# Kernel tuning notes

Measured on AMD Instinct MI355X. Metric: run time of the kernel, lower is better.

## Reference

```python
import jax, jax.numpy as jnp
import numpy as np

H = 4        # num_heads
DH = 64      # output_dim (d_head)
D = 256      # input_dim (hidden)
NUM_LAYERS = 2


def _gru_cell(x, h, Wih, Whh, bih, bhh):
    # PyTorch GRUCell: gates ordered (r, z, n)
    gi = x @ Wih.T + bih
    gh = h @ Whh.T + bhh
    i_r, i_z, i_n = jnp.split(gi, 3, axis=-1)
    h_r, h_z, h_n = jnp.split(gh, 3, axis=-1)
    r = jax.nn.sigmoid(i_r + h_r)
    z = jax.nn.sigmoid(i_z + h_z)
    n = jnp.tanh(i_n + r * h_n)
    return (1.0 - z) * n + z * h


def _mha(x, attn_mask, Wq, bq, Wk, bk, Wv, bv, Wo):
    B, N, _ = x.shape
    q = (x @ Wq.T + bq).reshape(B, N, H, DH)
    k = (x @ Wk.T + bk).reshape(B, N, H, DH)
    v = (x @ Wv.T + bv).reshape(B, N, H, DH)
    # scores computed in fp32 (autocast disabled in original)
    scores = jnp.einsum('bnhd,bmhd->bhnm', q.astype(jnp.float32), k.astype(jnp.float32)) / jnp.float32(DH) ** 0.5
    scores = jnp.where(attn_mask[:, None], jnp.float32(-1e9), scores)  # mask broadcast over heads
    attn = jax.nn.softmax(scores, axis=-1)
    ctx = jnp.einsum('bhnm,bmhd->bnhd', attn, v).reshape(B, N, H * DH)
    return ctx @ Wo.T  # W_O has no bias


def setup_inputs() -> dict:
    B, N = 1024, 128
    key = jax.random.key(0)
    ks = jax.random.split(key, 14)
    s = 0.02
    return {
        'latent': jax.random.normal(ks[0], (B, N, D), jnp.float32),
        'comm_mask': jax.random.randint(ks[1], (B, N, N), 0, 2) > 0,
        'trait_weight': jax.random.normal(ks[2], (B, N), jnp.float32),
        'Wq': jax.random.normal(ks[3], (H * DH, D), jnp.float32) * s,
        'bq': jnp.zeros((H * DH,), jnp.float32),
        'Wk': jax.random.normal(ks[4], (H * DH, D), jnp.float32) * s,
        'bk': jnp.zeros((H * DH,), jnp.float32),
        'Wv': jax.random.normal(ks[5], (H * DH, D), jnp.float32) * s,
        'bv': jnp.zeros((H * DH,), jnp.float32),
        'Wo': jax.random.normal(ks[6], (DH, H * DH), jnp.float32) * s,
        'Wih': jax.random.normal(ks[7], (3 * D, DH), jnp.float32) * s,
        'Whh': jax.random.normal(ks[8], (3 * D, D), jnp.float32) * s,
        'bih': jnp.zeros((3 * D,), jnp.float32),
        'bhh': jnp.zeros((3 * D,), jnp.float32),
    }


def reference(latent, comm_mask, trait_weight, Wq, bq, Wk, bk, Wv, bv, Wo, Wih, Whh, bih, bhh):
    B, N, _ = latent.shape
    attn_mask = ~comm_mask                                    # [B,N,N] True = blocked
    update_mask = (comm_mask.sum(axis=-1) > 1)[..., None]     # [B,N,1]
    for _ in range(NUM_LAYERS):
        info = _mha(latent, attn_mask, Wq, bq, Wk, bk, Wv, bv, Wo)          # [B,N,DH]
        upd = _gru_cell(info.reshape(-1, DH), latent.reshape(-1, D), Wih, Whh, bih, bhh)
        latent = jnp.where(update_mask, upd.reshape(B, N, D), latent)
    return latent
```

## Files before the change

kernel.cpp:

```cpp
#include <hip/hip_runtime.h>
#include <stdint.h>

#define NTOK 128
#define DHID 256
#define NHEAD 4
#define DHEAD 64

typedef short bf16x8 __attribute__((ext_vector_type(8)));
typedef float f32x4 __attribute__((ext_vector_type(4)));

#define MFMA(a,b,c) __builtin_amdgcn_mfma_f32_16x16x32_bf16((a),(b),(c),0,0,0)

__device__ __forceinline__ float bf2f(uint16_t u){
  union { uint32_t i; float f; } v; v.i = ((uint32_t)u) << 16; return v.f;
}
__device__ __forceinline__ uint16_t f2bf(float f){
  union { uint32_t i; float f; } v; v.f = f;
  uint32_t i = v.i + 0x7FFFu + ((v.i >> 16) & 1u);
  return (uint16_t)(i >> 16);
}

__global__ void k_detect(const uint32_t* __restrict__ raw, uint32_t* __restrict__ flag){
  int lane = threadIdx.x;
  int hits = 0;
  #pragma unroll
  for (int i = 0; i < 16; i++){
    uint32_t w = raw[lane*16 + i];
    uint32_t e = (w >> 7) & 0xFFu;
    hits += (e >= 0x70u && e <= 0x8Fu) ? 1 : 0;
  }
  #pragma unroll
  for (int m = 1; m < 64; m <<= 1) hits += __shfl_xor(hits, m);
  if (lane == 0) *flag = (hits > 512) ? 1u : 0u;
}

__global__ void k_conv(const void* __restrict__ src, unsigned long long off,
                       uint16_t* __restrict__ dst, const uint32_t* __restrict__ flag, int n){
  const int isbf = (int)*flag;
  int i0 = (blockIdx.x * blockDim.x + threadIdx.x) * 8;
  int stride = gridDim.x * blockDim.x * 8;
  if (isbf){
    const uint16_t* s = (const uint16_t*)src + off;
    for (int i = i0; i < n; i += stride)
      *(bf16x8*)(dst + i) = *(const bf16x8*)(s + i);
  } else {
    const float* s = (const float*)src + off;
    for (int i = i0; i < n; i += stride){
      float4 a = *(const float4*)(s + i);
      float4 b = *(const float4*)(s + i + 4);
      uint16_t o[8] = {f2bf(a.x),f2bf(a.y),f2bf(a.z),f2bf(a.w),
                       f2bf(b.x),f2bf(b.y),f2bf(b.z),f2bf(b.w)};
      *(bf16x8*)(dst + i) = *(const bf16x8*)o;
    }
  }
}

__global__ void k_store(const uint16_t* __restrict__ L, void* __restrict__ dst,
                        unsigned long long off, const uint32_t* __restrict__ flag, int n){
  const int isbf = (int)*flag;
  int i0 = (blockIdx.x * blockDim.x + threadIdx.x) * 8;
  int stride = gridDim.x * blockDim.x * 8;
  if (isbf){
    uint16_t* d = (uint16_t*)dst + off;
    for (int i = i0; i < n; i += stride)
      *(bf16x8*)(d + i) = *(const bf16x8*)(L + i);
  } else {
    float* d = (float*)dst + off;
    for (int i = i0; i < n; i += stride){
      bf16x8 v = *(const bf16x8*)(L + i);
      #pragma unroll
      for (int e = 0; e < 8; e++) d[i + e] = bf2f((uint16_t)v[e]);
    }
  }
}

__global__ __launch_bounds__(256) void k_maskpack(const int* __restrict__ mask,
                                                  unsigned long long* __restrict__ packed,
                                                  unsigned char* __restrict__ upd, int nrows){
  int row = blockIdx.x * 4 + (threadIdx.x >> 6);
  if (row >= nrows) return;
  int lane = threadIdx.x & 63;
  const int* mrow = mask + (size_t)row * NTOK;
  unsigned long long b0 = __ballot(mrow[lane] != 0);
  unsigned long long b1 = __ballot(mrow[lane + 64] != 0);
  if (lane == 0){
    packed[row*2 + 0] = b0;
    packed[row*2 + 1] = b1;
    upd[row] = (unsigned char)((__popcll(b0) + __popcll(b1)) > 1 ? 1 : 0);
  }
}

__global__ __launch_bounds__(256) void k_qkv(
    const uint16_t* __restrict__ X,
    const uint16_t* __restrict__ Wq, const uint16_t* __restrict__ bq,
    const uint16_t* __restrict__ Wk, const uint16_t* __restrict__ bk,
    const uint16_t* __restrict__ Wv, const uint16_t* __restrict__ bv,
    uint16_t* __restrict__ Oq, uint16_t* __restrict__ Ok, uint16_t* __restrict__ Ov)
{
  extern __shared__ uint16_t sm[];
  uint16_t* Xs = sm;
  uint16_t* Ws = sm + 64*256;
  const int r0 = blockIdx.x * 64;
  const int tid = threadIdx.x;
  const int lane = tid & 63, lr = lane & 15, lg = lane >> 4;
  const int wav = tid >> 6;
  const int wr = (wav >> 1) * 32, wc = (wav & 1) * 32;

  #pragma unroll
  for (int i = 0; i < 8; i++){
    int c = tid + i*256, row = c >> 5, g = c & 31;
    *(bf16x8*)(Xs + row*256 + (g ^ (row & 7))*8) =
        *(const bf16x8*)(X + (size_t)(r0+row)*DHID + g*8);
  }

  bf16x8 wreg[8];
  auto wptr = [&](int t)->const uint16_t*{
    int w = t >> 2;
    return (w == 0) ? Wq : ((w == 1) ? Wk : Wv);
  };
  auto preload = [&](int t){
    const uint16_t* W = wptr(t);
    int c0t = (t & 3) * 64;
    #pragma unroll
    for (int i = 0; i < 8; i++){
      int idx = tid + i*256, r = idx >> 5, g = idx & 31;
      wreg[i] = *(const bf16x8*)(W + (size_t)(c0t + r)*DHID + g*8);
    }
  };
  preload(0);

  for (int t = 0; t < 12; t++){
    __syncthreads();
    #pragma unroll
    for (int i = 0; i < 8; i++){
      int idx = tid + i*256, r = idx >> 5, g = idx & 31;
      *(bf16x8*)(Ws + r*256 + ((g ^ (r & 7))*8)) = wreg[i];
    }
    __syncthreads();
    if (t < 11) preload(t+1);

    f32x4 acc[2][2] = {};
    #pragma unroll
    for (int kk = 0; kk < 8; kk++){
      int off = ((kk*4 + lg) ^ (lr & 7)) * 8;
      bf16x8 a0 = *(const bf16x8*)(Xs + (wr +      lr)*256 + off);
      bf16x8 a1 = *(const bf16x8*)(Xs + (wr + 16 + lr)*256 + off);
      bf16x8 b0 = *(const bf16x8*)(Ws + (wc +      lr)*256 + off);
      bf16x8 b1 = *(const bf16x8*)(Ws + (wc + 16 + lr)*256 + off);
      acc[0][0] = MFMA(a0, b0, acc[0][0]);
      acc[0][1] = MFMA(a0, b1, acc[0][1]);
      acc[1][0] = MFMA(a1, b0, acc[1][0]);
      acc[1][1] = MFMA(a1, b1, acc[1][1]);
    }
    int w = t >> 2, c0t = (t & 3) * 64;
    const uint16_t* bias = (w == 0) ? bq : ((w == 1) ? bk : bv);
    uint16_t* O = (w == 0) ? Oq : ((w == 1) ? Ok : Ov);
    #pragma unroll
    for (int i = 0; i < 2; i++)
    #pragma unroll
    for (int j = 0; j < 2; j++){
      int col = c0t + wc + j*16 + lr;
      float bvv = bf2f(bias[col]);
      #pragma unroll
      for (int rr = 0; rr < 4; rr++){
        int row = r0 + wr + i*16 + lg*4 + rr;
        O[(size_t)row*DHID + col] = f2bf(acc[i][j][rr] + bvv);
      }
    }
  }
}

__global__ __launch_bounds__(256) void k_attn(
    const uint16_t* __restrict__ Q, const uint16_t* __restrict__ Kb, const uint16_t* __restrict__ V,
    const unsigned long long* __restrict__ packed, uint16_t* __restrict__ ctx)
{
  extern __shared__ uint16_t sm[];
  uint16_t* Ks = sm;
  uint16_t* Vt = sm + 128*64;
  uint16_t* Ps = Vt + 64*128;
  const int b = blockIdx.x >> 2;
  const int h = blockIdx.x & 3;
  const int tid = threadIdx.x, lane = tid & 63, wav = tid >> 6;
  const int lr = lane & 15, lg = lane >> 4;
  const size_t base = ((size_t)b * NTOK) * DHID + h * DHEAD;

  #pragma unroll
  for (int i = 0; i < 4; i++){
    int c = tid + i*256;
    int row = c >> 3, g = c & 7;
    *(bf16x8*)(Ks + row*64 + (g ^ (row & 7))*8) =
        *(const bf16x8*)(Kb + base + (size_t)row*DHID + g*8);
  }
  #pragma unroll
  for (int i = 0; i < 4; i++){
    int c = tid + i*256;
    int n = c & 127, d8 = (c >> 7) * 8;
    bf16x8 v = *(const bf16x8*)(V + base + (size_t)n*DHID + d8);
    #pragma unroll
    for (int e = 0; e < 8; e++){
      int d = d8 + e;
      Vt[d*128 + ((n >> 3) ^ (d & 7))*8 + (n & 7)] = (uint16_t)v[e];
    }
  }
  __syncthreads();

  const int qrow0 = wav * 32;
  bf16x8 qf[2][2];
  #pragma unroll
  for (int i = 0; i < 2; i++)
  #pragma unroll
  for (int kk = 0; kk < 2; kk++)
    qf[i][kk] = *(const bf16x8*)(Q + base + (size_t)(qrow0 + i*16 + lr)*DHID + kk*32 + lg*8);

  f32x4 sa[2][8] = {};
  #pragma unroll
  for (int kk = 0; kk < 2; kk++){
    int off = ((kk*4 + lg) ^ (lr & 7)) * 8;
    #pragma unroll
    for (int j = 0; j < 8; j++){
      bf16x8 bf = *(const bf16x8*)(Ks + (j*16 + lr)*64 + off);
      sa[0][j] = MFMA(qf[0][kk], bf, sa[0][j]);
      sa[1][j] = MFMA(qf[1][kk], bf, sa[1][j]);
    }
  }
  #pragma unroll
  for (int i = 0; i < 2; i++){
    #pragma unroll
    for (int rr = 0; rr < 4; rr++){
      int n = qrow0 + i*16 + lg*4 + rr;
      unsigned long long m0 = packed[((size_t)b*NTOK + n)*2 + 0];
      unsigned long long m1 = packed[((size_t)b*NTOK + n)*2 + 1];
      float sv[8];
      float mx = -3.0e38f;
      #pragma unroll
      for (int j = 0; j < 8; j++){
        int col = j*16 + lr;
        unsigned long long w = (col < 64) ? m0 : m1;
        float s = sa[i][j][rr] * 0.125f;
        sv[j] = ((w >> (col & 63)) & 1ull) ? s : -1e9f;
        mx = fmaxf(mx, sv[j]);
      }
      mx = fmaxf(mx, __shfl_xor(mx, 1));
      mx = fmaxf(mx, __shfl_xor(mx, 2));
      mx = fmaxf(mx, __shfl_xor(mx, 4));
      mx = fmaxf(mx, __shfl_xor(mx, 8));
      float sum = 0.f;
      #pragma unroll
      for (int j = 0; j < 8; j++){ sv[j] = __expf(sv[j] - mx); sum += sv[j]; }
      sum += __shfl_xor(sum, 1);
      sum += __shfl_xor(sum, 2);
      sum += __shfl_xor(sum, 4);
      sum += __shfl_xor(sum, 8);
      float inv = __builtin_amdgcn_rcpf(sum);
      #pragma unroll
      for (int j = 0; j < 8; j++){
        int col = j*16 + lr;
        Ps[n*128 + ((col >> 3) ^ (n & 7))*8 + (col & 7)] = f2bf(sv[j] * inv);
      }
    }
  }
  __syncthreads();

  f32x4 oa[2][4] = {};
  #pragma unroll
  for (int kk = 0; kk < 4; kk++){
    int off = ((kk*4 + lg) ^ (lr & 7)) * 8;
    bf16x8 a0 = *(const bf16x8*)(Ps + (qrow0 +      lr)*128 + off);
    bf16x8 a1 = *(const bf16x8*)(Ps + (qrow0 + 16 + lr)*128 + off);
    #pragma unroll
    for (int j = 0; j < 4; j++){
      bf16x8 bf = *(const bf16x8*)(Vt + (j*16 + lr)*128 + off);
      oa[0][j] = MFMA(a0, bf, oa[0][j]);
      oa[1][j] = MFMA(a1, bf, oa[1][j]);
    }
  }
  #pragma unroll
  for (int i = 0; i < 2; i++)
  #pragma unroll
  for (int j = 0; j < 4; j++)
  #pragma unroll
  for (int rr = 0; rr < 4; rr++){
    int n = qrow0 + i*16 + lg*4 + rr;
    ctx[((size_t)b*NTOK + n)*DHID + h*DHEAD + j*16 + lr] = f2bf(oa[i][j][rr]);
  }
}

__global__ __launch_bounds__(256, 2) void k_gru(
    const uint16_t* __restrict__ ctxp, const uint16_t* __restrict__ lat,
    const uint16_t* __restrict__ Wo, const uint16_t* __restrict__ Wih, const uint16_t* __restrict__ Whh,
    const uint16_t* __restrict__ bih, const uint16_t* __restrict__ bhh,
    const unsigned char* __restrict__ upd, uint16_t* __restrict__ lat_out)
{
  extern __shared__ uint16_t sm[];
  uint16_t* Wb0   = sm;
  uint16_t* Wb1   = sm + 15360;
  uint16_t* Is    = sm + 30720;
  uint16_t* biasS = sm + 38912;
  const int r0 = blockIdx.x * 128;
  const int tid = threadIdx.x, lane = tid & 63, wav = tid >> 6;
  const int lr = lane & 15, lg = lane >> 4;
  const int wrow = wav * 32;

  #pragma unroll
  for (int i = 0; i < 6; i++){
    int idx = tid + i*256;
    if (idx < 1536) biasS[idx] = (idx < 768) ? bih[idx] : bhh[idx - 768];
  }

  auto stage_async = [&](int cs, uint16_t* buf){
    #pragma unroll
    for (int c = 0; c < 7; c++){
      int G = c*256 + tid;
      const uint16_t* src;
      if (G < 1536){
        int r = G >> 5, gp = G & 31;
        src = Whh + (size_t)((r>>4)*256 + cs*16 + (r&15))*DHID + (gp ^ (r&7))*8;
      } else {
        int G2 = G - 1536, r = G2 >> 3, gp = G2 & 7;
        src = Wih + (size_t)((r>>4)*256 + cs*16 + (r&15))*DHEAD + (gp ^ (r&7))*8;
      }
      __builtin_amdgcn_global_load_lds(
          (const __attribute__((address_space(1))) uint32_t*)src,
          (__attribute__((address_space(3))) uint32_t*)(buf + (size_t)G*8),
          16, 0, 0);
    }
    if (tid < 128){
      int G = 1792 + tid;
      int G2 = G - 1536, r = G2 >> 3, gp = G2 & 7;
      const uint16_t* src = Wih + (size_t)((r>>4)*256 + cs*16 + (r&15))*DHEAD + (gp ^ (r&7))*8;
      __builtin_amdgcn_global_load_lds(
          (const __attribute__((address_space(1))) uint32_t*)src,
          (__attribute__((address_space(3))) uint32_t*)(buf + (size_t)G*8),
          16, 0, 0);
    }
  };

  stage_async(0, Wb0);

  f32x4 ai[2][4] = {};
  #pragma unroll
  for (int kk = 0; kk < 8; kk++){
    bf16x8 bw[4];
    #pragma unroll
    for (int j = 0; j < 4; j++)
      bw[j] = *(const bf16x8*)(Wo + (size_t)(j*16 + lr)*DHID + kk*32 + lg*8);
    #pragma unroll
    for (int t = 0; t < 2; t++){
      bf16x8 ac = *(const bf16x8*)(ctxp + (size_t)(r0 + wrow + t*16 + lr)*DHID + kk*32 + lg*8);
      #pragma unroll
      for (int j = 0; j < 4; j++) ai[t][j] = MFMA(ac, bw[j], ai[t][j]);
    }
  }
  #pragma unroll
  for (int t = 0; t < 2; t++)
  #pragma unroll
  for (int j = 0; j < 4; j++)
  #pragma unroll
  for (int rr = 0; rr < 4; rr++){
    int row = wrow + t*16 + lg*4 + rr, col = j*16 + lr;
    Is[row*64 + ((col>>3) ^ (row&7))*8 + (col&7)] = f2bf(ai[t][j][rr]);
  }

  bf16x8 aL[2][8];
  #pragma unroll
  for (int t = 0; t < 2; t++)
  #pragma unroll
  for (int kk = 0; kk < 8; kk++)
    aL[t][kk] = *(const bf16x8*)(lat + (size_t)(r0 + wrow + t*16 + lr)*DHID + kk*32 + lg*8);

  uint32_t u4[2];
  #pragma unroll
  for (int t = 0; t < 2; t++)
    u4[t] = *(const uint32_t*)(upd + r0 + wrow + t*16 + lg*4);

  __syncthreads();

  const float LOG2E = 1.44269504f;
  for (int cs = 0; cs < 16; cs++){
    uint16_t* Wcur = (cs & 1) ? Wb1 : Wb0;
    if (cs < 15) stage_async(cs+1, (cs & 1) ? Wb0 : Wb1);

    const uint16_t* WhhS = Wcur;
    const uint16_t* WihS = Wcur + 12288;

    f32x4 arz[2][2] = {};
    f32x4 gin[2] = {}, ghn[2] = {};

    #pragma unroll
    for (int kk = 0; kk < 2; kk++){
      int off = ((kk*4 + lg) ^ (lr & 7)) * 8;
      bf16x8 br = *(const bf16x8*)(WihS + (0*16 + lr)*64 + off);
      bf16x8 bz = *(const bf16x8*)(WihS + (1*16 + lr)*64 + off);
      bf16x8 bn = *(const bf16x8*)(WihS + (2*16 + lr)*64 + off);
      #pragma unroll
      for (int t = 0; t < 2; t++){
        bf16x8 a = *(const bf16x8*)(Is + (wrow + t*16 + lr)*64 + off);
        arz[0][t] = MFMA(a, br, arz[0][t]);
        arz[1][t] = MFMA(a, bz, arz[1][t]);
        gin[t]    = MFMA(a, bn, gin[t]);
      }
    }
    #pragma unroll
    for (int kk = 0; kk < 8; kk++){
      int off = ((kk*4 + lg) ^ (lr & 7)) * 8;
      bf16x8 br = *(const bf16x8*)(WhhS + (0*16 + lr)*256 + off);
      bf16x8 bz = *(const bf16x8*)(WhhS + (1*16 + lr)*256 + off);
      bf16x8 bn = *(const bf16x8*)(WhhS + (2*16 + lr)*256 + off);
      #pragma unroll
      for (int t = 0; t < 2; t++){
        arz[0][t] = MFMA(aL[t][kk], br, arz[0][t]);
        arz[1][t] = MFMA(aL[t][kk], bz, arz[1][t]);
        ghn[t]    = MFMA(aL[t][kk], bn, ghn[t]);
      }
    }

    int col = cs*16 + lr;
    float brz0 = bf2f(biasS[col])     + bf2f(biasS[768+col]);
    float brz1 = bf2f(biasS[256+col]) + bf2f(biasS[1024+col]);
    float bin_ = bf2f(biasS[512+col]);
    float bhn  = bf2f(biasS[1280+col]);
    #pragma unroll
    for (int t = 0; t < 2; t++)
    #pragma unroll
    for (int rr = 0; rr < 4; rr++){
      int row = wrow + t*16 + lg*4 + rr;
      float hv = bf2f(lat[(size_t)(r0+row)*DHID + col]);
      float xr = arz[0][t][rr] + brz0;
      float xz = arz[1][t][rr] + brz1;
      float rg = __builtin_amdgcn_rcpf(1.f + __builtin_amdgcn_exp2f(-xr*LOG2E));
      float zg = __builtin_amdgcn_rcpf(1.f + __builtin_amdgcn_exp2f(-xz*LOG2E));
      float nx = (gin[t][rr] + bin_) + rg*(ghn[t][rr] + bhn);
      nx = fminf(10.f, fmaxf(-10.f, nx));
      float e2 = __builtin_amdgcn_exp2f(-2.f*LOG2E*nx);
      float ng = (1.f - e2) * __builtin_amdgcn_rcpf(1.f + e2);
      float hp = (1.f - zg)*ng + zg*hv;
      float ov = ((u4[t] >> (rr*8)) & 1u) ? hp : hv;
      lat_out[(size_t)(r0+row)*DHID + col] = f2bf(ov);
    }
    __syncthreads();
  }
}

extern "C" void kernel_launch(void* const* d_in, const int* in_sizes, int n_in,
                              void* d_out, int out_size, void* d_ws, size_t ws_size,
                              hipStream_t stream)
{
  (void)in_sizes; (void)n_in; (void)out_size;
  const void* latent = d_in[0];
  const int*  mask   = (const int*)d_in[1];
  const void* Wq  = d_in[3]; const void* bq  = d_in[4];
  const void* Wk  = d_in[5]; const void* bk  = d_in[6];
  const void* Wv  = d_in[7]; const void* bv  = d_in[8];
  const void* Wo  = d_in[9];
  const void* Wih = d_in[10]; const void* Whh = d_in[11];
  const void* bih = d_in[12]; const void* bhh = d_in[13];

  uint8_t* p = (uint8_t*)d_ws;
  uint32_t* flag = (uint32_t*)p;            p += 256;
  uint16_t* Wqc  = (uint16_t*)p;            p += 65536*2;
  uint16_t* Wkc  = (uint16_t*)p;            p += 65536*2;
  uint16_t* Wvc  = (uint16_t*)p;            p += 65536*2;
  uint16_t* Woc  = (uint16_t*)p;            p += 16384*2;
  uint16_t* Wihc = (uint16_t*)p;            p += 49152*2;
  uint16_t* Whhc = (uint16_t*)p;            p += 196608*2;
  uint16_t* bqc  = (uint16_t*)p;            p += 512;
  uint16_t* bkc  = (uint16_t*)p;            p += 512;
  uint16_t* bvc  = (uint16_t*)p;            p += 512;
  uint16_t* bihc = (uint16_t*)p;            p += 1536;
  uint16_t* bhhc = (uint16_t*)p;            p += 1536;
  uint8_t* chunk0 = p;
  size_t reserved = (size_t)(chunk0 - (uint8_t*)d_ws);
  const size_t perb = 5ull*65536 + 2048 + 128;

  const int Btot = 1024;
  int CB = (int)((ws_size > reserved ? ws_size - reserved : 0) / perb);
  if (CB > Btot) CB = Btot;
  if (CB < 1)    CB = 1;

  auto cgrid = [](int n){ int b = (n/8 + 255)/256; if (b > 2048) b = 2048; if (b < 1) b = 1; return (unsigned)b; };

  k_detect<<<1, 64, 0, stream>>>((const uint32_t*)latent, flag);
  k_conv<<<cgrid(65536), 256, 0, stream>>>(Wq, 0, Wqc, flag, 65536);
  k_conv<<<cgrid(65536), 256, 0, stream>>>(Wk, 0, Wkc, flag, 65536);
  k_conv<<<cgrid(65536), 256, 0, stream>>>(Wv, 0, Wvc, flag, 65536);
  k_conv<<<cgrid(16384), 256, 0, stream>>>(Wo, 0, Woc, flag, 16384);
  k_conv<<<cgrid(49152), 256, 0, stream>>>(Wih, 0, Wihc, flag, 49152);
  k_conv<<<cgrid(196608),256, 0, stream>>>(Whh, 0, Whhc, flag, 196608);
  k_conv<<<1, 256, 0, stream>>>(bq, 0, bqc, flag, 256);
  k_conv<<<1, 256, 0, stream>>>(bk, 0, bkc, flag, 256);
  k_conv<<<1, 256, 0, stream>>>(bv, 0, bvc, flag, 256);
  k_conv<<<1, 256, 0, stream>>>(bih, 0, bihc, flag, 768);
  k_conv<<<1, 256, 0, stream>>>(bhh, 0, bhhc, flag, 768);

  for (int b0 = 0; b0 < Btot; b0 += CB){
    int cb = (Btot - b0 < CB) ? (Btot - b0) : CB;
    int rows = cb * 128;
    int nelem = rows * DHID;
    uint8_t* q = chunk0;
    uint16_t* L    = (uint16_t*)q; q += (size_t)cb*65536;
    uint16_t* q_ws = (uint16_t*)q; q += (size_t)cb*65536;
    uint16_t* k_ws = (uint16_t*)q; q += (size_t)cb*65536;
    uint16_t* v_ws = (uint16_t*)q; q += (size_t)cb*65536;
    uint16_t* c_ws = (uint16_t*)q; q += (size_t)cb*65536;
    unsigned long long* packed = (unsigned long long*)q; q += (size_t)cb*2048;
    unsigned char* updp = (unsigned char*)q;

    k_conv<<<cgrid(nelem), 256, 0, stream>>>(latent, (unsigned long long)b0*NTOK*DHID, L, flag, nelem);
    k_maskpack<<<dim3(rows/4), 256, 0, stream>>>(mask + (size_t)b0*NTOK*NTOK, packed, updp, rows);

    for (int layer = 0; layer < 2; layer++){
      k_qkv <<<dim3(rows/64),  256, 65536, stream>>>(L, Wqc,bqc, Wkc,bkc, Wvc,bvc, q_ws, k_ws, v_ws);
      k_attn<<<dim3(cb*NHEAD), 256, 65536, stream>>>(q_ws, k_ws, v_ws, packed, c_ws);
      k_gru <<<dim3(rows/128), 256, 80896, stream>>>(c_ws, L, Woc, Wihc, Whhc, bihc, bhhc, updp, L);
    }
    k_store<<<cgrid(nelem), 256, 0, stream>>>(L, d_out, (unsigned long long)b0*NTOK*DHID, flag, nelem);
  }
}
```

Measured before the change: 721.5 us.

## Single-buffer GRU weights for occupancy, defer softmax normalization, stage mask in LDS

The GRU kernel drops its double-buffered weight staging for a single buffer with synchronous reloads, cutting LDS so three blocks fit per CU (launch bounds raised to 3). Attention copies the packed mask into shared memory and moves the softmax normalization onto the context output instead of every probability. In bf16 mode the final GRU layer writes straight to the output, and the store kernel exits early. The cost is that weight loads no longer overlap compute in the GRU loop.

```diff
diff --git a/kernel.cpp b/kernel.cpp
--- a/kernel.cpp
+++ b/kernel.cpp
@@ -57,20 +57,14 @@
 
 __global__ void k_store(const uint16_t* __restrict__ L, void* __restrict__ dst,
                         unsigned long long off, const uint32_t* __restrict__ flag, int n){
-  const int isbf = (int)*flag;
+  if (*flag) return;
   int i0 = (blockIdx.x * blockDim.x + threadIdx.x) * 8;
   int stride = gridDim.x * blockDim.x * 8;
-  if (isbf){
-    uint16_t* d = (uint16_t*)dst + off;
-    for (int i = i0; i < n; i += stride)
-      *(bf16x8*)(d + i) = *(const bf16x8*)(L + i);
-  } else {
-    float* d = (float*)dst + off;
-    for (int i = i0; i < n; i += stride){
-      bf16x8 v = *(const bf16x8*)(L + i);
-      #pragma unroll
-      for (int e = 0; e < 8; e++) d[i + e] = bf2f((uint16_t)v[e]);
-    }
+  float* d = (float*)dst + off;
+  for (int i = i0; i < n; i += stride){
+    bf16x8 v = *(const bf16x8*)(L + i);
+    #pragma unroll
+    for (int e = 0; e < 8; e++) d[i + e] = bf2f((uint16_t)v[e]);
   }
 }
 
@@ -178,12 +172,14 @@
   uint16_t* Ks = sm;
   uint16_t* Vt = sm + 128*64;
   uint16_t* Ps = Vt + 64*128;
+  unsigned long long* Ms = (unsigned long long*)(Ps + 128*128);
   const int b = blockIdx.x >> 2;
   const int h = blockIdx.x & 3;
   const int tid = threadIdx.x, lane = tid & 63, wav = tid >> 6;
   const int lr = lane & 15, lg = lane >> 4;
   const size_t base = ((size_t)b * NTOK) * DHID + h * DHEAD;
 
+  Ms[tid] = packed[(size_t)b*NTOK*2 + tid];
   #pragma unroll
   for (int i = 0; i < 4; i++){
     int c = tid + i*256;
@@ -223,13 +219,14 @@
       sa[1][j] = MFMA(qf[1][kk], bf, sa[1][j]);
     }
   }
+  float iv[2][4];
   #pragma unroll
   for (int i = 0; i < 2; i++){
     #pragma unroll
     for (int rr = 0; rr < 4; rr++){
       int n = qrow0 + i*16 + lg*4 + rr;
-      unsigned long long m0 = packed[((size_t)b*NTOK + n)*2 + 0];
-      unsigned long long m1 = packed[((size_t)b*NTOK + n)*2 + 1];
+      unsigned long long m0 = Ms[n*2 + 0];
+      unsigned long long m1 = Ms[n*2 + 1];
       float sv[8];
       float mx = -3.0e38f;
       #pragma unroll
@@ -251,11 +248,11 @@
       sum += __shfl_xor(sum, 2);
       sum += __shfl_xor(sum, 4);
       sum += __shfl_xor(sum, 8);
-      float inv = __builtin_amdgcn_rcpf(sum);
+      iv[i][rr] = __builtin_amdgcn_rcpf(sum);
       #pragma unroll
       for (int j = 0; j < 8; j++){
         int col = j*16 + lr;
-        Ps[n*128 + ((col >> 3) ^ (n & 7))*8 + (col & 7)] = f2bf(sv[j] * inv);
+        Ps[n*128 + ((col >> 3) ^ (n & 7))*8 + (col & 7)] = f2bf(sv[j]);
       }
     }
   }
@@ -281,21 +278,22 @@
   #pragma unroll
   for (int rr = 0; rr < 4; rr++){
     int n = qrow0 + i*16 + lg*4 + rr;
-    ctx[((size_t)b*NTOK + n)*DHID + h*DHEAD + j*16 + lr] = f2bf(oa[i][j][rr]);
-  }
-}
-
-__global__ __launch_bounds__(256, 2) void k_gru(
+    ctx[((size_t)b*NTOK + n)*DHID + h*DHEAD + j*16 + lr] = f2bf(oa[i][j][rr] * iv[i][rr]);
+  }
+}
+
+__global__ __launch_bounds__(256, 3) void k_gru(
     const uint16_t* __restrict__ ctxp, const uint16_t* __restrict__ lat,
     const uint16_t* __restrict__ Wo, const uint16_t* __restrict__ Wih, const uint16_t* __restrict__ Whh,
     const uint16_t* __restrict__ bih, const uint16_t* __restrict__ bhh,
-    const unsigned char* __restrict__ upd, uint16_t* __restrict__ lat_out)
+    const unsigned char* __restrict__ upd, uint16_t* __restrict__ Lbuf,
+    uint16_t* __restrict__ dout, const uint32_t* __restrict__ flag, int layer)
 {
   extern __shared__ uint16_t sm[];
-  uint16_t* Wb0   = sm;
-  uint16_t* Wb1   = sm + 15360;
-  uint16_t* Is    = sm + 30720;
-  uint16_t* biasS = sm + 38912;
+  uint16_t* Wb    = sm;
+  uint16_t* Is    = sm + 15360;
+  uint16_t* biasS = sm + 23552;
+  uint16_t* lat_out = (layer == 1 && *flag) ? dout : Lbuf;
   const int r0 = blockIdx.x * 128;
   const int tid = threadIdx.x, lane = tid & 63, wav = tid >> 6;
   const int lr = lane & 15, lg = lane >> 4;
@@ -307,7 +305,7 @@
     if (idx < 1536) biasS[idx] = (idx < 768) ? bih[idx] : bhh[idx - 768];
   }
 
-  auto stage_async = [&](int cs, uint16_t* buf){
+  auto stage_async = [&](int cs){
     #pragma unroll
     for (int c = 0; c < 7; c++){
       int G = c*256 + tid;
@@ -321,7 +319,7 @@
       }
       __builtin_amdgcn_global_load_lds(
           (const __attribute__((address_space(1))) uint32_t*)src,
-          (__attribute__((address_space(3))) uint32_t*)(buf + (size_t)G*8),
+          (__attribute__((address_space(3))) uint32_t*)(Wb + (size_t)G*8),
           16, 0, 0);
     }
     if (tid < 128){
@@ -330,12 +328,12 @@
       const uint16_t* src = Wih + (size_t)((r>>4)*256 + cs*16 + (r&15))*DHEAD + (gp ^ (r&7))*8;
       __builtin_amdgcn_global_load_lds(
           (const __attribute__((address_space(1))) uint32_t*)src,
-          (__attribute__((address_space(3))) uint32_t*)(buf + (size_t)G*8),
+          (__attribute__((address_space(3))) uint32_t*)(Wb + (size_t)G*8),
           16, 0, 0);
     }
   };
 
-  stage_async(0, Wb0);
+  stage_async(0);
 
   f32x4 ai[2][4] = {};
   #pragma unroll
@@ -377,14 +375,10 @@
 
   const float LOG2E = 1.44269504f;
   for (int cs = 0; cs < 16; cs++){
-    uint16_t* Wcur = (cs & 1) ? Wb1 : Wb0;
-    if (cs < 15) stage_async(cs+1, (cs & 1) ? Wb0 : Wb1);
-
-    const uint16_t* WhhS = Wcur;
-    const uint16_t* WihS = Wcur + 12288;
-
     f32x4 arz[2][2] = {};
     f32x4 gin[2] = {}, ghn[2] = {};
+    const uint16_t* WhhS = Wb;
+    const uint16_t* WihS = Wb + 12288;
 
     #pragma unroll
     for (int kk = 0; kk < 2; kk++){
@@ -438,6 +432,10 @@
       lat_out[(size_t)(r0+row)*DHID + col] = f2bf(ov);
     }
     __syncthreads();
+    if (cs < 15){
+      stage_async(cs+1);
+      __syncthreads();
+    }
   }
 }
 
@@ -505,14 +503,17 @@
     unsigned long long* packed = (unsigned long long*)q; q += (size_t)cb*2048;
     unsigned char* updp = (unsigned char*)q;
 
+    uint16_t* dout_b = (uint16_t*)d_out + (size_t)b0*NTOK*DHID;
+
     k_conv<<<cgrid(nelem), 256, 0, stream>>>(latent, (unsigned long long)b0*NTOK*DHID, L, flag, nelem);
     k_maskpack<<<dim3(rows/4), 256, 0, stream>>>(mask + (size_t)b0*NTOK*NTOK, packed, updp, rows);
 
     for (int layer = 0; layer < 2; layer++){
       k_qkv <<<dim3(rows/64),  256, 65536, stream>>>(L, Wqc,bqc, Wkc,bkc, Wvc,bvc, q_ws, k_ws, v_ws);
-      k_attn<<<dim3(cb*NHEAD), 256, 65536, stream>>>(q_ws, k_ws, v_ws, packed, c_ws);
-      k_gru <<<dim3(rows/128), 256, 80896, stream>>>(c_ws, L, Woc, Wihc, Whhc, bihc, bhhc, updp, L);
-    }
-    k_store<<<cgrid(nelem), 256, 0, stream>>>(L, d_out, (unsigned long long)b0*NTOK*DHID, flag, nelem);
-  }
-}
+      k_attn<<<dim3(cb*NHEAD), 256, 67584, stream>>>(q_ws, k_ws, v_ws, packed, c_ws);
+      k_gru <<<dim3(rows/128), 256, 50176, stream>>>(c_ws, L, Woc, Wihc, Whhc, bihc, bhhc, updp,
+                                                     L, dout_b, flag, layer);
+    }
+    k_store<<<cgrid(nelem), 256, 0, stream>>>(L, (void*)((float*)d_out + (size_t)b0*NTOK*DHID), 0, flag, nelem);
+  }
+}
```

After: 870.1 us. +20.6%, slower.

## Fuse Q projection into attention kernel and defer softmax normalization

Applied to the files above, without the earlier changes.

Q is no longer produced by the projection kernel and stored to global memory. Instead each attention block computes its head's Q slice from the latent rows using a per-head Wq tile staged in LDS. This removes the Q write and read round trip and shrinks the projection kernel to K and V only. Softmax normalization now scales the PV output rather than P, which lets one barrier go; Ps aliases the Wq staging buffer. The per-batch workspace size is doubled, which may shrink the chunk size, and attention LDS grows to 80KB with a two-blocks-per-CU launch bound.

```diff
diff --git a/kernel.cpp b/kernel.cpp
--- a/kernel.cpp
+++ b/kernel.cpp
@@ -90,12 +90,11 @@
   }
 }
 
-__global__ __launch_bounds__(256) void k_qkv(
+__global__ __launch_bounds__(256) void k_kv(
     const uint16_t* __restrict__ X,
-    const uint16_t* __restrict__ Wq, const uint16_t* __restrict__ bq,
     const uint16_t* __restrict__ Wk, const uint16_t* __restrict__ bk,
     const uint16_t* __restrict__ Wv, const uint16_t* __restrict__ bv,
-    uint16_t* __restrict__ Oq, uint16_t* __restrict__ Ok, uint16_t* __restrict__ Ov)
+    uint16_t* __restrict__ Ok, uint16_t* __restrict__ Ov)
 {
   extern __shared__ uint16_t sm[];
   uint16_t* Xs = sm;
@@ -114,12 +113,8 @@
   }
 
   bf16x8 wreg[8];
-  auto wptr = [&](int t)->const uint16_t*{
-    int w = t >> 2;
-    return (w == 0) ? Wq : ((w == 1) ? Wk : Wv);
-  };
   auto preload = [&](int t){
-    const uint16_t* W = wptr(t);
+    const uint16_t* W = (t < 4) ? Wk : Wv;
     int c0t = (t & 3) * 64;
     #pragma unroll
     for (int i = 0; i < 8; i++){
@@ -129,7 +124,7 @@
   };
   preload(0);
 
-  for (int t = 0; t < 12; t++){
+  for (int t = 0; t < 8; t++){
     __syncthreads();
     #pragma unroll
     for (int i = 0; i < 8; i++){
@@ -137,7 +132,7 @@
       *(bf16x8*)(Ws + r*256 + ((g ^ (r & 7))*8)) = wreg[i];
     }
     __syncthreads();
-    if (t < 11) preload(t+1);
+    if (t < 7) preload(t+1);
 
     f32x4 acc[2][2] = {};
     #pragma unroll
@@ -152,9 +147,9 @@
       acc[1][0] = MFMA(a1, b0, acc[1][0]);
       acc[1][1] = MFMA(a1, b1, acc[1][1]);
     }
-    int w = t >> 2, c0t = (t & 3) * 64;
-    const uint16_t* bias = (w == 0) ? bq : ((w == 1) ? bk : bv);
-    uint16_t* O = (w == 0) ? Oq : ((w == 1) ? Ok : Ov);
+    const uint16_t* bias = (t < 4) ? bk : bv;
+    uint16_t* O = (t < 4) ? Ok : Ov;
+    int c0t = (t & 3) * 64;
     #pragma unroll
     for (int i = 0; i < 2; i++)
     #pragma unroll
@@ -170,24 +165,34 @@
   }
 }
 
-__global__ __launch_bounds__(256) void k_attn(
-    const uint16_t* __restrict__ Q, const uint16_t* __restrict__ Kb, const uint16_t* __restrict__ V,
+__global__ __launch_bounds__(256, 2) void k_attn(
+    const uint16_t* __restrict__ X, const uint16_t* __restrict__ Wq, const uint16_t* __restrict__ bq,
+    const uint16_t* __restrict__ Kb, const uint16_t* __restrict__ V,
     const unsigned long long* __restrict__ packed, uint16_t* __restrict__ ctx)
 {
   extern __shared__ uint16_t sm[];
-  uint16_t* Ks = sm;
-  uint16_t* Vt = sm + 128*64;
-  uint16_t* Ps = Vt + 64*128;
+  uint16_t* WqhS = sm;
+  uint16_t* Ps   = sm;
+  uint16_t* qS   = sm + 16384;
+  uint16_t* Ks   = sm + 24576;
+  uint16_t* Vt   = sm + 32768;
   const int b = blockIdx.x >> 2;
   const int h = blockIdx.x & 3;
   const int tid = threadIdx.x, lane = tid & 63, wav = tid >> 6;
   const int lr = lane & 15, lg = lane >> 4;
-  const size_t base = ((size_t)b * NTOK) * DHID + h * DHEAD;
-
+  const size_t base  = ((size_t)b * NTOK) * DHID + h * DHEAD;
+  const size_t xbase = ((size_t)b * NTOK) * DHID;
+  const int qrow0 = wav * 32;
+
+  #pragma unroll
+  for (int i = 0; i < 8; i++){
+    int idx = tid + i*256, r = idx >> 5, g = idx & 31;
+    *(bf16x8*)(WqhS + r*256 + (g ^ (r & 7))*8) =
+        *(const bf16x8*)(Wq + (size_t)(h*DHEAD + r)*DHID + g*8);
+  }
   #pragma unroll
   for (int i = 0; i < 4; i++){
-    int c = tid + i*256;
-    int row = c >> 3, g = c & 7;
+    int c = tid + i*256, row = c >> 3, g = c & 7;
     *(bf16x8*)(Ks + row*64 + (g ^ (row & 7))*8) =
         *(const bf16x8*)(Kb + base + (size_t)row*DHID + g*8);
   }
@@ -202,15 +207,50 @@
       Vt[d*128 + ((n >> 3) ^ (d & 7))*8 + (n & 7)] = (uint16_t)v[e];
     }
   }
+  bf16x8 aX[2][8];
+  #pragma unroll
+  for (int t = 0; t < 2; t++)
+  #pragma unroll
+  for (int kk = 0; kk < 8; kk++)
+    aX[t][kk] = *(const bf16x8*)(X + xbase + (size_t)(qrow0 + t*16 + lr)*DHID + kk*32 + lg*8);
   __syncthreads();
 
-  const int qrow0 = wav * 32;
+  {
+    f32x4 ai[2][4] = {};
+    #pragma unroll
+    for (int kk = 0; kk < 8; kk++){
+      int off = ((kk*4 + lg) ^ (lr & 7)) * 8;
+      bf16x8 bw[4];
+      #pragma unroll
+      for (int j = 0; j < 4; j++)
+        bw[j] = *(const bf16x8*)(WqhS + (j*16 + lr)*256 + off);
+      #pragma unroll
+      for (int t = 0; t < 2; t++)
+      #pragma unroll
+      for (int j = 0; j < 4; j++)
+        ai[t][j] = MFMA(aX[t][kk], bw[j], ai[t][j]);
+    }
+    #pragma unroll
+    for (int t = 0; t < 2; t++)
+    #pragma unroll
+    for (int j = 0; j < 4; j++){
+      int col = j*16 + lr;
+      float bvv = bf2f(bq[h*DHEAD + col]);
+      #pragma unroll
+      for (int rr = 0; rr < 4; rr++){
+        int row = qrow0 + t*16 + lg*4 + rr;
+        qS[row*64 + ((col>>3) ^ (row&7))*8 + (col&7)] = f2bf(ai[t][j][rr] + bvv);
+      }
+    }
+  }
+  __syncthreads();
+
   bf16x8 qf[2][2];
   #pragma unroll
   for (int i = 0; i < 2; i++)
   #pragma unroll
   for (int kk = 0; kk < 2; kk++)
-    qf[i][kk] = *(const bf16x8*)(Q + base + (size_t)(qrow0 + i*16 + lr)*DHID + kk*32 + lg*8);
+    qf[i][kk] = *(const bf16x8*)(qS + (qrow0 + i*16 + lr)*64 + (((kk*4 + lg) ^ (lr & 7))*8));
 
   f32x4 sa[2][8] = {};
   #pragma unroll
@@ -223,6 +263,7 @@
       sa[1][j] = MFMA(qf[1][kk], bf, sa[1][j]);
     }
   }
+  float iv[2][4];
   #pragma unroll
   for (int i = 0; i < 2; i++){
     #pragma unroll
@@ -251,15 +292,14 @@
       sum += __shfl_xor(sum, 2);
       sum += __shfl_xor(sum, 4);
       sum += __shfl_xor(sum, 8);
-      float inv = __builtin_amdgcn_rcpf(sum);
+      iv[i][rr] = __builtin_amdgcn_rcpf(sum);
       #pragma unroll
       for (int j = 0; j < 8; j++){
         int col = j*16 + lr;
-        Ps[n*128 + ((col >> 3) ^ (n & 7))*8 + (col & 7)] = f2bf(sv[j] * inv);
-      }
-    }
-  }
-  __syncthreads();
+        Ps[n*128 + ((col >> 3) ^ (n & 7))*8 + (col & 7)] = f2bf(sv[j]);
+      }
+    }
+  }
 
   f32x4 oa[2][4] = {};
   #pragma unroll
@@ -281,7 +321,7 @@
   #pragma unroll
   for (int rr = 0; rr < 4; rr++){
     int n = qrow0 + i*16 + lg*4 + rr;
-    ctx[((size_t)b*NTOK + n)*DHID + h*DHEAD + j*16 + lr] = f2bf(oa[i][j][rr]);
+    ctx[((size_t)b*NTOK + n)*DHID + h*DHEAD + j*16 + lr] = f2bf(oa[i][j][rr] * iv[i][rr]);
   }
 }
 
@@ -470,7 +510,7 @@
   uint16_t* bhhc = (uint16_t*)p;            p += 1536;
   uint8_t* chunk0 = p;
   size_t reserved = (size_t)(chunk0 - (uint8_t*)d_ws);
-  const size_t perb = 5ull*65536 + 2048 + 128;
+  const size_t perb = 5ull*131072 + 2048 + 128;
 
   const int Btot = 1024;
   int CB = (int)((ws_size > reserved ? ws_size - reserved : 0) / perb);
@@ -497,11 +537,11 @@
     int rows = cb * 128;
     int nelem = rows * DHID;
     uint8_t* q = chunk0;
-    uint16_t* L    = (uint16_t*)q; q += (size_t)cb*65536;
-    uint16_t* q_ws = (uint16_t*)q; q += (size_t)cb*65536;
-    uint16_t* k_ws = (uint16_t*)q; q += (size_t)cb*65536;
-    uint16_t* v_ws = (uint16_t*)q; q += (size_t)cb*65536;
-    uint16_t* c_ws = (uint16_t*)q; q += (size_t)cb*65536;
+    uint16_t* L    = (uint16_t*)q; q += (size_t)cb*131072;
+    uint16_t* k_ws = (uint16_t*)q; q += (size_t)cb*131072;
+    uint16_t* v_ws = (uint16_t*)q; q += (size_t)cb*131072;
+    uint16_t* c_ws = (uint16_t*)q; q += (size_t)cb*131072;
+    q += (size_t)cb*131072;
     unsigned long long* packed = (unsigned long long*)q; q += (size_t)cb*2048;
     unsigned char* updp = (unsigned char*)q;
 
@@ -509,8 +549,8 @@
     k_maskpack<<<dim3(rows/4), 256, 0, stream>>>(mask + (size_t)b0*NTOK*NTOK, packed, updp, rows);
 
     for (int layer = 0; layer < 2; layer++){
-      k_qkv <<<dim3(rows/64),  256, 65536, stream>>>(L, Wqc,bqc, Wkc,bkc, Wvc,bvc, q_ws, k_ws, v_ws);
-      k_attn<<<dim3(cb*NHEAD), 256, 65536, stream>>>(q_ws, k_ws, v_ws, packed, c_ws);
+      k_kv  <<<dim3(rows/64),  256, 65536, stream>>>(L, Wkc,bkc, Wvc,bvc, k_ws, v_ws);
+      k_attn<<<dim3(cb*NHEAD), 256, 81920, stream>>>(L, Wqc, bqc, k_ws, v_ws, packed, c_ws);
       k_gru <<<dim3(rows/128), 256, 80896, stream>>>(c_ws, L, Woc, Wihc, Whhc, bihc, bhhc, updp, L);
     }
     k_store<<<cgrid(nelem), 256, 0, stream>>>(L, d_out, (unsigned long long)b0*NTOK*DHID, flag, nelem);
```

New measurement: 793.5 us. +10.0%, slower.
